# Optimization experiments

Measured on AMD Instinct MI355X. Metric: run time of the kernel, lower is better.

The kernel has to match this reference:

```python
import jax, jax.numpy as jnp
import numpy as np

N = 2000   # nodes
K = 16     # receptive-field size (exact degree incl. self-loop)
C_IN = 16  # input_feats
H = 16     # hidden_size
NC = 18    # num_contractions


def setup_inputs() -> dict:
    key = jax.random.key(0)
    k1, k2, k3, k4, k5, k6 = jax.random.split(key, 6)
    # adjacency with exactly K ones per row (self-loop + K-1 distinct random nbrs)
    u = jax.random.uniform(k1, (N, N))
    u = u.at[jnp.arange(N), jnp.arange(N)].set(-1.0)  # force self into top-K
    nbrs = jnp.argsort(u, axis=1)[:, :K]
    adj = jnp.zeros((N, N), jnp.float32).at[jnp.arange(N)[:, None], nbrs].set(1.0)
    X = jax.random.normal(k2, (N, C_IN), jnp.float32)
    scale = 0.1
    W1 = scale * jax.random.normal(k3, (H, NC * C_IN), jnp.float32)
    b1 = jnp.zeros((H,), jnp.float32)
    W2 = scale * jax.random.normal(k4, (H, NC * H), jnp.float32)
    b2 = jnp.zeros((H,), jnp.float32)
    fc_w = scale * jax.random.normal(k5, (1, 2 * H + C_IN), jnp.float32)
    fc_b = scale * jax.random.normal(k6, (1,), jnp.float32)
    return {"X": X, "adj": adj, "W1": W1, "b1": b1, "W2": W2, "b2": b2,
            "fc_w": fc_w, "fc_b": fc_b}


def _neighbors(adj):
    # each row has exactly K ones -> top_k returns their indices
    _, idx = jax.lax.top_k(adj, K)
    return jnp.sort(idx, axis=1)  # (N, K)


def _contract18(T):
    # T: (n, m, a, b, c) stacked promoted neighbor tensors; 18 contractions 3rd->2nd order
    n, k, _, _, c = T.shape
    tr = lambda M: jnp.swapaxes(M, 1, 2)
    s0, s1, s2 = T.sum(1), T.sum(2), T.sum(3)           # single-index sums
    d0 = jnp.einsum('ixxbc->ixbc', T)                    # diag m=a
    d1 = jnp.einsum('ixaxc->ixac', T)                    # diag m=b
    d2 = jnp.einsum('imyyc->imyc', T)                    # diag a=b
    outs = []
    for M in (s0, s1, s2, d0, d1, d2):
        outs.append(M)
        outs.append(tr(M))                               # 12 so far
    v0, v1, v2 = T.sum((2, 3)), T.sum((1, 3)), T.sum((1, 2))  # double sums -> vectors
    for v in (v0, v1, v2):
        outs.append(jnp.broadcast_to(v[:, :, None, :], (n, k, k, c)))  # rows
        outs.append(jnp.broadcast_to(v[:, None, :, :], (n, k, k, c)))  # cols
    return jnp.concatenate(outs, axis=-1)                # (n, k, k, 18c)


def _forward(X, adj, W1, b1, W2, b2, fc_w, fc_b):
    nbrs = _neighbors(adj)                               # (N, K)
    nbrs_nb = nbrs[nbrs]                                 # (N, K, K)
    # chi[i,m,a,b] = 1 iff a-th member of P_i equals b-th member of P_{nbrs[i,m]}
    chi = (nbrs[:, None, :, None] == nbrs_nb[:, :, None, :]).astype(X.dtype)  # (N,K,K,K)
    # F0: first->second order promotion (features on the diagonal of P_i x P_i)
    F0 = jnp.einsum('ab,iac->iabc', jnp.eye(K, dtype=X.dtype), X[nbrs])  # (N,K,K,C_IN)

    def step(F, W, b):
        Fn = F[nbrs]                                     # (N, m, p, q, c)
        tmp = jnp.einsum('imap,impqc->imaqc', chi, Fn)
        T = jnp.einsum('imaqc,imbq->imabc', tmp, chi)    # promoted + stacked (N,m,a,b,c)
        C = _contract18(T)                               # (N, a, b, 18c)
        return jax.nn.relu(jnp.einsum('iabk,hk->iabh', C, W) + b)

    F1 = step(F0, W1, b1)
    F2 = step(F1, W2, b2)
    g = jnp.concatenate([F0.sum((0, 1, 2)), F1.sum((0, 1, 2)), F2.sum((0, 1, 2))])
    return g @ fc_w.T + fc_b                             # (n_outputs,)


def reference(X, adj, W1, b1, W2, b2, fc_w, fc_b):
    return _forward(X, adj, W1, b1, W2, b2, fc_w, fc_b)
```

## Files before the change

kernel.cpp:

```cpp
#include <hip/hip_runtime.h>

#define NN 2000

typedef _Float16 halfx8 __attribute__((ext_vector_type(8)));
typedef float floatx4 __attribute__((ext_vector_type(4)));

#define LBAR() asm volatile("s_waitcnt lgkmcnt(0)\n\ts_barrier" ::: "memory")

__device__ __forceinline__ unsigned char to_fp8(float v) {
    return (unsigned char)(__builtin_amdgcn_cvt_pk_fp8_f32(v, 0.f, 0, false) & 0xff);
}

__global__ void build_nbrs_k(const float* __restrict__ adj,
                             int* __restrict__ nbrs,
                             float* __restrict__ gsum) {
    int i = blockIdx.x;
    int lane = threadIdx.x;
    if (i == 0 && lane == 0) {
        gsum[0] = 0.0f;
        ((unsigned*)gsum)[1] = 0u;
    }
    const float4* row = (const float4*)(adj + (size_t)i * NN);
    float4 v[8];
#pragma unroll
    for (int c = 0; c < 8; ++c) {
        int idx4 = c * 64 + lane;
        if (idx4 < 500) v[c] = row[idx4];
        else            v[c] = make_float4(0.f, 0.f, 0.f, 0.f);
    }
    int base = 0;
#pragma unroll
    for (int c = 0; c < 8; ++c) {
        unsigned nib = (v[c].x > 0.5f ? 1u : 0u) | (v[c].y > 0.5f ? 2u : 0u) |
                       (v[c].z > 0.5f ? 4u : 0u) | (v[c].w > 0.5f ? 8u : 0u);
        unsigned long long b0 = __ballot(nib & 1u);
        unsigned long long b1 = __ballot(nib & 2u);
        unsigned long long b2 = __ballot(nib & 4u);
        unsigned long long b3 = __ballot(nib & 8u);
        unsigned long long below = (1ull << lane) - 1ull;
        int pos = base + __popcll(b0 & below) + __popcll(b1 & below) +
                         __popcll(b2 & below) + __popcll(b3 & below);
        int col0 = c * 256 + lane * 4;
        if (nib & 1u) { nbrs[i * 16 + pos] = col0;     ++pos; }
        if (nib & 2u) { nbrs[i * 16 + pos] = col0 + 1; ++pos; }
        if (nib & 4u) { nbrs[i * 16 + pos] = col0 + 2; ++pos; }
        if (nib & 8u) { nbrs[i * 16 + pos] = col0 + 3; ++pos; }
        base += __popcll(b0) + __popcll(b1) + __popcll(b2) + __popcll(b3);
    }
}

__global__ void build_map_prep_k(const int* __restrict__ nbrs,
                                 signed char* __restrict__ map8,
                                 signed char* __restrict__ imp8,
                                 int4* __restrict__ aux,
                                 const float* __restrict__ W1,
                                 const float* __restrict__ W2,
                                 unsigned char* __restrict__ Wpk8,
                                 _Float16* __restrict__ Wpk16) {
    if (blockIdx.x >= 125) {
        int idx = (blockIdx.x - 125) * 256 + threadIdx.x;
        if (idx >= 10240) return;
        if (idx < 6144) {
            int stage = idx / 3072;
            int r = idx % 3072;
            int c = r / 512;
            int r2 = r % 512;
            int L = r2 >> 3, jj = r2 & 7;
            int q = L >> 4, h = L & 15;
            int k = q * 8 + jj;
            const int bA[6] = {2, 6, 10, 3, 7, 11};
            const int bB[6] = {4, 8, -1, 5, 9, -1};
            int tb = (k < 16) ? bA[c] : bB[c];
            int ci = k & 15;
            const float* W = stage ? W2 : W1;
            float val = (tb < 0) ? 0.f : W[h * 288 + tb * 16 + ci];
            Wpk8[idx] = to_fp8(val);
        } else {
            int id2 = idx - 6144;
            int stage = id2 / 2048;
            int r = id2 % 2048;
            int c = r / 512;
            int r2 = r % 512;
            int L = r2 >> 3, jj = r2 & 7;
            int q = L >> 4, h = L & 15;
            int k = q * 8 + jj;
            const int bA[4] = {0, 14, 1, 15};
            const int bB[4] = {12, 16, 13, 17};
            int tb = (k < 16) ? bA[c] : bB[c];
            int ci = k & 15;
            const float* W = stage ? W2 : W1;
            float val = W[h * 288 + tb * 16 + ci];
            Wpk16[id2] = (_Float16)val;
        }
        return;
    }
    int idx = blockIdx.x * 256 + threadIdx.x;
    if (idx >= NN * 16) return;
    int i = idx >> 4;
    int m = idx & 15;
    int j = nbrs[idx];
    const int4* pi = (const int4*)(nbrs + (size_t)i * 16);
    const int4* pj = (const int4*)(nbrs + (size_t)j * 16);
    int4 A = pi[0], Bq = pi[1], C = pi[2], D = pi[3];
    int4 E = pj[0], F = pj[1], G = pj[2], H = pj[3];
    int ni[16] = {A.x,A.y,A.z,A.w, Bq.x,Bq.y,Bq.z,Bq.w, C.x,C.y,C.z,C.w, D.x,D.y,D.z,D.w};
    int nj[16] = {E.x,E.y,E.z,E.w, F.x,F.y,F.z,F.w, G.x,G.y,G.z,G.w, H.x,H.y,H.z,H.w};

    int mp[16];
    unsigned long long lo = 0, hi = 0;
#pragma unroll
    for (int a = 0; a < 16; ++a) {
        int r = -1;
#pragma unroll
        for (int p = 0; p < 16; ++p)
            if (nj[p] == ni[a]) r = p;
        mp[a] = r;
        unsigned long long b = (unsigned long long)(r & 0xff);
        if (a < 8) lo |= b << (8 * a); else hi |= b << (8 * (a - 8));
    }
    uint4 pk;
    pk.x = (unsigned)lo; pk.y = (unsigned)(lo >> 32);
    pk.z = (unsigned)hi; pk.w = (unsigned)(hi >> 32);
    *(uint4*)(map8 + ((size_t)idx << 4)) = pk;
    lo = 0; hi = 0;
#pragma unroll
    for (int p = 0; p < 16; ++p) {
        int r = -1;
#pragma unroll
        for (int a = 0; a < 16; ++a)
            if (ni[a] == nj[p]) r = a;
        unsigned long long b = (unsigned long long)(r & 0xff);
        if (p < 8) lo |= b << (8 * p); else hi |= b << (8 * (p - 8));
    }
    pk.x = (unsigned)lo; pk.y = (unsigned)(lo >> 32);
    pk.z = (unsigned)hi; pk.w = (unsigned)(hi >> 32);
    *(uint4*)(imp8 + ((size_t)idx << 4)) = pk;

    unsigned vm = 0;
    int a1 = -1, a2 = -1, pa1 = 0, pa2 = 0;
#pragma unroll
    for (int a = 0; a < 16; ++a) {
        if (mp[a] >= 0) {
            vm |= (1u << a);
            if (a1 < 0)      { a1 = a; pa1 = mp[a]; }
            else if (a2 < 0) { a2 = a; pa2 = mp[a]; }
        }
    }
    int ms = 0;
#pragma unroll
    for (int a = 0; a < 16; ++a)
        if (ni[a] == i) ms = a;
    int4 av;
    av.x = j;
    av.y = (a1 & 0xff) | ((pa1 & 0xff) << 8) | ((a2 & 0xff) << 16) | ((pa2 & 0xff) << 24);
    av.z = (int)(vm | ((unsigned)(mp[m] & 0xff) << 16) | ((unsigned)(ms & 0xff) << 24));
    av.w = 0;
    aux[idx] = av;
}

template <int DIAG>
__global__ __launch_bounds__(256, 3)
void step_k(const float* __restrict__ Fp,
            const float* __restrict__ Xp,
            const unsigned char* __restrict__ Wpk8s,
            const _Float16* __restrict__ Wpk16s,
            const float* __restrict__ bias,
            const signed char* __restrict__ map8,
            const signed char* __restrict__ imp8,
            const int4* __restrict__ auxp,
            float* __restrict__ Fout,
            float* __restrict__ gp0,
            float* __restrict__ gp) {
    __shared__ __attribute__((aligned(16))) float S0[16][16][16];
    __shared__ __attribute__((aligned(16))) unsigned char MAP8[5][16][16][16];
    __shared__ __attribute__((aligned(16))) float V0f[16][16];
    __shared__ __attribute__((aligned(16))) float V1f[16][16];
    __shared__ __attribute__((aligned(16))) float V2f[16][16];
    __shared__ __attribute__((aligned(16))) float S1f[16][16];

    const int i = blockIdx.x;
    const int t = threadIdx.x;
    const int u = t >> 4;
    const int l = t & 15;
    const int lane = t & 63, q = lane >> 4, h = lane & 15, wv = t >> 6;

    int4 av = auxp[i * 16 + u];
    uint4 imv = *(const uint4*)(imp8 + ((size_t)(i * 16 + u) << 4));
    float bv = bias[l];
    const int j = av.x;
    const int a1 = (int)(signed char)(av.y & 0xff);
    const int pa1 = (av.y >> 8) & 0xff;
    const int a2 = (int)(signed char)((av.y >> 16) & 0xff);
    const int pa2 = (av.y >> 24) & 0xff;
    const unsigned vm = (unsigned)(av.z & 0xffff);
    const int pmm = (av.z >> 16) & 0xff;
    const int ms = (av.z >> 24) & 0xff;

    float frow[16], fcol[16], xv = 0.f;
    if (DIAG) {
        xv = Xp[(size_t)j * 16 + l];
    } else {
        const float* Fi = Fp + (size_t)i * 4096;
#pragma unroll
        for (int b = 0; b < 16; ++b) frow[b] = Fi[(u * 16 + b) * 16 + l];
#pragma unroll
        for (int a = 0; a < 16; ++a) fcol[a] = Fi[(a * 16 + u) * 16 + l];
    }

    float R1[16], R2[16];
    if (!DIAG && u != ms) {
        const float* P1 = Fp + (((size_t)j * 256 + pa1 * 16) * 16) + l;
#pragma unroll
        for (int p = 0; p < 16; ++p) R1[p] = P1[p * 16];
        if (a2 >= 0) {
            const float* P2 = Fp + (((size_t)j * 256 + pa2 * 16) * 16) + l;
#pragma unroll
            for (int p = 0; p < 16; ++p) R2[p] = P2[p * 16];
        }
    }
    long Bf8[6];
    {
        const long* Wq8 = (const long*)Wpk8s;
#pragma unroll
        for (int c = 0; c < 6; ++c) Bf8[c] = Wq8[c * 64 + lane];
    }
    halfx8 Bf16[4];
    {
        const halfx8* Wq16 = (const halfx8*)Wpk16s;
#pragma unroll
        for (int c = 0; c < 4; ++c) Bf16[c] = Wq16[c * 64 + lane];
    }

    if (u != ms) {
        uint4 z = {0u, 0u, 0u, 0u};
#pragma unroll
        for (int k = 0; k < 5; ++k)
            *(uint4*)&MAP8[k][u][l][0] = z;
    }
    if (DIAG) {
        S1f[u][l] = xv;
        V1f[u][l] = xv;
        V2f[u][l] = xv;
#pragma unroll
        for (int b = 0; b < 16; ++b) S0[u][b][l] = (b == u) ? xv : 0.f;
        unsigned char x8 = to_fp8(xv);
        MAP8[0][ms][u][l] = x8;
        MAP8[1][ms][u][l] = x8;
        unsigned char dz = (u == ms) ? x8 : (unsigned char)0;
        MAP8[2][ms][u][l] = dz;
        MAP8[3][ms][u][l] = dz;
        MAP8[4][ms][u][l] = x8;
    } else {
        float s2 = 0.f, a10 = 0.f, a8 = 0.f;
#pragma unroll
        for (int b = 0; b < 16; ++b) {
            float v = frow[b];
            s2 += v;
            S0[u][b][l] = v;
            if (b == u)  a10 = v;
            if (b == ms) a8 = v;
        }
        float s1 = 0.f, a6 = 0.f;
#pragma unroll
        for (int a = 0; a < 16; ++a) {
            float v = fcol[a];
            s1 += v;
            if (a == ms) a6 = v;
        }
        S1f[u][l] = s2;
        V1f[u][l] = s2;
        V2f[u][l] = s1;
        MAP8[0][ms][u][l] = to_fp8(s1);
        MAP8[1][ms][u][l] = to_fp8(s2);
        MAP8[2][ms][u][l] = to_fp8(a6);
        MAP8[3][ms][u][l] = to_fp8(a8);
        MAP8[4][ms][u][l] = to_fp8(a10);
    }
    LBAR();

    if (u != ms) {
        const int m = u;
        float v0acc = 0.f;
        if (DIAG) {
#pragma unroll
            for (int a = 0; a < 16; ++a) {
                if ((vm >> a) & 1u) {
                    float v = S1f[a][l];
                    v0acc += v;
                    atomicAdd(&S0[a][a][l], v);
                    atomicAdd(&V1f[a][l], v);
                    atomicAdd(&V2f[a][l], v);
                    unsigned char v8 = to_fp8(v);
                    MAP8[0][m][a][l] = v8;
                    MAP8[1][m][a][l] = v8;
                    MAP8[4][m][a][l] = v8;
                    if (a == m) { MAP8[2][m][m][l] = v8; MAP8[3][m][m][l] = v8; }
                }
            }
        } else {
            float colacc[16];
#pragma unroll
            for (int p = 0; p < 16; ++p) colacc[p] = 0.f;
            auto process = [&](int a, int pa, const float (&vr)[16]) {
                float rowacc = 0.f, a8v = 0.f, a10v = 0.f;
                const bool am = (a == m);
#pragma unroll
                for (int p = 0; p < 16; ++p) {
                    float v = vr[p];
                    if (p == pmm) a8v = v;
                    if (p == pa)  a10v = v;
                    unsigned dw = (p < 4) ? imv.x : ((p < 8) ? imv.y : ((p < 12) ? imv.z : imv.w));
                    int b = (int)(signed char)((dw >> (8 * (p & 3))) & 0xffu);
                    if (b >= 0) {
                        rowacc += v;
                        colacc[p] += v;
                        atomicAdd(&S0[a][b][l], v);
                        atomicAdd(&V2f[b][l], v);
                        if (am) MAP8[2][m][b][l] = to_fp8(v);
                    }
                }
                v0acc += rowacc;
                atomicAdd(&V1f[a][l], rowacc);
                MAP8[1][m][a][l] = to_fp8(rowacc);
                MAP8[3][m][a][l] = to_fp8(a8v);
                MAP8[4][m][a][l] = to_fp8(a10v);
            };
            process(a1, pa1, R1);
            if (a2 >= 0) process(a2, pa2, R2);
            unsigned rm = vm & ~(1u << a1);
            if (a2 >= 0) rm &= ~(1u << a2);
            if (rm) {
                uint4 mpq = *(const uint4*)(map8 + ((size_t)(i * 16 + u) << 4));
                do {
                    int a = __builtin_ctz(rm); rm &= rm - 1;
                    unsigned dw = (a & 8) ? ((a & 4) ? mpq.w : mpq.z) : ((a & 4) ? mpq.y : mpq.x);
                    int pa = (int)(signed char)((dw >> (8 * (a & 3))) & 0xffu);
                    float RT[16];
                    const float* P3 = Fp + (((size_t)j * 256 + pa * 16) * 16) + l;
#pragma unroll
                    for (int p = 0; p < 16; ++p) RT[p] = P3[p * 16];
                    process(a, pa, RT);
                } while (rm);
            }
#pragma unroll
            for (int p = 0; p < 16; ++p) {
                unsigned dw = (p < 4) ? imv.x : ((p < 8) ? imv.y : ((p < 12) ? imv.z : imv.w));
                int b = (int)(signed char)((dw >> (8 * (p & 3))) & 0xffu);
                if (b >= 0) MAP8[0][m][b][l] = to_fp8(colacc[p]);
            }
        }
        V0f[m][l] = v0acc;
    } else {
        float v0s = 0.f;
#pragma unroll
        for (int b = 0; b < 16; ++b) v0s += S1f[b][l];
        V0f[ms][l] = v0s;
        if (DIAG) gp0[l * 2048 + i] = v0s;
    }

    floatx4 acc1[4], acc2[4];
#pragma unroll
    for (int tt = 0; tt < 4; ++tt) {
        acc1[tt] = (floatx4){0.f, 0.f, 0.f, 0.f};
        acc2[tt] = (floatx4){0.f, 0.f, 0.f, 0.f};
    }
    const int wbase = wv * 4;
    {
        const int off8 = (q & 1) * 8;
        const unsigned char* mA = (q < 2) ? &MAP8[0][0][0][0] : &MAP8[1][0][0][0];
        const unsigned char* mB = (q < 2) ? &MAP8[2][0][0][0] : &MAP8[3][0][0][0];
        const unsigned char* mC = &MAP8[4][0][0][0];
#pragma unroll
        for (int tt = 0; tt < 4; ++tt) {
            const int x = wbase + tt;
            const int base = x * 256 + h * 16 + off8;
            long f0 = *(const long*)(mA + base);
            long f1 = *(const long*)(mB + base);
            long f2 = (q < 2) ? *(const long*)(mC + base) : 0L;
            acc1[tt] = __builtin_amdgcn_mfma_f32_16x16x32_fp8_fp8(f0, Bf8[0], acc1[tt], 0, 0, 0);
            acc1[tt] = __builtin_amdgcn_mfma_f32_16x16x32_fp8_fp8(f1, Bf8[1], acc1[tt], 0, 0, 0);
            acc1[tt] = __builtin_amdgcn_mfma_f32_16x16x32_fp8_fp8(f2, Bf8[2], acc1[tt], 0, 0, 0);
            acc2[tt] = __builtin_amdgcn_mfma_f32_16x16x32_fp8_fp8(f0, Bf8[3], acc2[tt], 0, 0, 0);
            acc2[tt] = __builtin_amdgcn_mfma_f32_16x16x32_fp8_fp8(f1, Bf8[4], acc2[tt], 0, 0, 0);
            acc2[tt] = __builtin_amdgcn_mfma_f32_16x16x32_fp8_fp8(f2, Bf8[5], acc2[tt], 0, 0, 0);
        }
    }
    LBAR();

    auto cvt8a = [](const float* p) -> halfx8 {
        float4 va = *(const float4*)p, vb = *(const float4*)(p + 4);
        halfx8 r;
        r[0] = (_Float16)va.x; r[1] = (_Float16)va.y; r[2] = (_Float16)va.z; r[3] = (_Float16)va.w;
        r[4] = (_Float16)vb.x; r[5] = (_Float16)vb.y; r[6] = (_Float16)vb.z; r[7] = (_Float16)vb.w;
        return r;
    };
#pragma unroll
    for (int tt = 0; tt < 4; ++tt) {
        const int x = wbase + tt;
        halfx8 p3, p4;
        if (q < 2) {
            p3 = cvt8a(&S0[x][h][q * 8]);
            p4 = cvt8a(&V1f[x][q * 8]);
        } else {
            const int c0 = (q - 2) * 8;
            p3 = cvt8a(&V0f[x][c0]);
            p4 = cvt8a(&V2f[x][c0]);
        }
        acc1[tt] = __builtin_amdgcn_mfma_f32_16x16x32_f16(p3, Bf16[0], acc1[tt], 0, 0, 0);
        acc1[tt] = __builtin_amdgcn_mfma_f32_16x16x32_f16(p4, Bf16[1], acc1[tt], 0, 0, 0);
        acc2[tt] = __builtin_amdgcn_mfma_f32_16x16x32_f16(p3, Bf16[2], acc2[tt], 0, 0, 0);
        acc2[tt] = __builtin_amdgcn_mfma_f32_16x16x32_f16(p4, Bf16[3], acc2[tt], 0, 0, 0);
    }

    float* P2f = (float*)&MAP8[0][0][0][0];
#pragma unroll
    for (int tt = 0; tt < 4; ++tt) {
        const int x = wbase + tt;
#pragma unroll
        for (int r = 0; r < 4; ++r)
            P2f[(x * 16 + (q * 4 + r)) * 17 + h] = acc2[tt][r];
    }
    LBAR();

    float gpart = 0.f;
#pragma unroll
    for (int tt = 0; tt < 4; ++tt) {
        const int x = wbase + tt;
#pragma unroll
        for (int r = 0; r < 4; ++r) {
            const int y = q * 4 + r;
            float val = acc1[tt][r] + P2f[(y * 16 + x) * 17 + h] + bv;
            val = fmaxf(val, 0.f);
            gpart += val;
            if (Fout) Fout[(size_t)i * 4096 + (x * 16 + y) * 16 + h] = val;
        }
    }
    gpart += __shfl_xor(gpart, 16, 64);
    gpart += __shfl_xor(gpart, 32, 64);
    if (lane < 16) gp[h * 8192 + i * 4 + wv] = gpart;
}

__global__ void reduce_fin_k(const float* __restrict__ parts,
                             float* __restrict__ gsum,
                             const float* __restrict__ fcw,
                             const float* __restrict__ fcb,
                             float* __restrict__ out) {
    int r = blockIdx.x;
    const float* p;
    int cnt4;
    if (r < 16)      { p = parts + r * 2048;                    cnt4 = 500;  }
    else if (r < 32) { p = parts + 32768 + (r - 16) * 8192;     cnt4 = 2000; }
    else             { p = parts + 163840 + (r - 32) * 8192;    cnt4 = 2000; }
    const float4* p4 = (const float4*)p;
    int t = threadIdx.x;
    float s = 0.f;
    for (int n = t; n < cnt4; n += 256) {
        float4 v = p4[n];
        s += v.x + v.y + v.z + v.w;
    }
#pragma unroll
    for (int off = 32; off > 0; off >>= 1) s += __shfl_xor(s, off, 64);
    __shared__ float wsum[4];
    if ((t & 63) == 0) wsum[t >> 6] = s;
    __syncthreads();
    if (t == 0) {
        float tot = wsum[0] + wsum[1] + wsum[2] + wsum[3];
        atomicAdd(&gsum[0], tot * fcw[r]);
        __threadfence();
        unsigned old = atomicAdd((unsigned*)gsum + 1, 1u);
        if (old == 47u) {
            float acc = atomicAdd(&gsum[0], 0.0f);
            out[0] = acc + fcb[0];
        }
    }
}

extern "C" void kernel_launch(void* const* d_in, const int* in_sizes, int n_in,
                              void* d_out, int out_size, void* d_ws, size_t ws_size,
                              hipStream_t stream) {
    const float* X   = (const float*)d_in[0];
    const float* adj = (const float*)d_in[1];
    const float* W1  = (const float*)d_in[2];
    const float* b1  = (const float*)d_in[3];
    const float* W2  = (const float*)d_in[4];
    const float* b2  = (const float*)d_in[5];
    const float* fcw = (const float*)d_in[6];
    const float* fcb = (const float*)d_in[7];
    float* out = (float*)d_out;
    char* ws = (char*)d_ws;

    float*         gsum  = (float*)(ws + 0);
    int*           nbrs  = (int*)(ws + 1024);
    signed char*   map8  = (signed char*)(ws + 129280);
    signed char*   imp8  = (signed char*)(ws + 641280);
    int4*          aux   = (int4*)(ws + 1153280);
    float*         parts = (float*)(ws + 1665280);
    unsigned char* Wpk8  = (unsigned char*)(ws + 2844928);
    _Float16*      Wpk16 = (_Float16*)(ws + 2851072);
    float*         F1    = (float*)(ws + 2859264);

    build_nbrs_k<<<NN, 64, 0, stream>>>(adj, nbrs, gsum);
    build_map_prep_k<<<165, 256, 0, stream>>>(nbrs, map8, imp8, aux, W1, W2, Wpk8, Wpk16);
    step_k<1><<<NN, 256, 0, stream>>>(nullptr, X, Wpk8, Wpk16, b1, map8, imp8, aux, F1,
                                      parts, parts + 32768);
    step_k<0><<<NN, 256, 0, stream>>>(F1, X, Wpk8 + 3072, Wpk16 + 2048, b2, map8, imp8, aux,
                                      nullptr, nullptr, parts + 163840);
    reduce_fin_k<<<48, 256, 0, stream>>>(parts, gsum, fcw, fcb, out);
}
```

Measured before the change: 145.9 us.

## Fold neighbor-map construction into step kernels and merge weight prep into nbrs kernel

Removes the separate map-building kernel. The weight-packing work moves into the adjacency-scan kernel as extra blocks, and each step kernel now computes its own neighbor-overlap maps (map, inverse map, first matches, self index) with wavefront ballots and shuffles. This saves one launch and the global writes and reads of the map8, imp8 and aux buffers. In exchange both step kernels redo the matching work and carry extra registers, which may affect occupancy under the launch bounds.

```diff
diff --git a/kernel.cpp b/kernel.cpp
--- a/kernel.cpp
+++ b/kernel.cpp
@@ -13,52 +13,15 @@
 
 __global__ void build_nbrs_k(const float* __restrict__ adj,
                              int* __restrict__ nbrs,
-                             float* __restrict__ gsum) {
+                             float* __restrict__ gsum,
+                             const float* __restrict__ W1,
+                             const float* __restrict__ W2,
+                             unsigned char* __restrict__ Wpk8,
+                             _Float16* __restrict__ Wpk16) {
     int i = blockIdx.x;
     int lane = threadIdx.x;
-    if (i == 0 && lane == 0) {
-        gsum[0] = 0.0f;
-        ((unsigned*)gsum)[1] = 0u;
-    }
-    const float4* row = (const float4*)(adj + (size_t)i * NN);
-    float4 v[8];
-#pragma unroll
-    for (int c = 0; c < 8; ++c) {
-        int idx4 = c * 64 + lane;
-        if (idx4 < 500) v[c] = row[idx4];
-        else            v[c] = make_float4(0.f, 0.f, 0.f, 0.f);
-    }
-    int base = 0;
-#pragma unroll
-    for (int c = 0; c < 8; ++c) {
-        unsigned nib = (v[c].x > 0.5f ? 1u : 0u) | (v[c].y > 0.5f ? 2u : 0u) |
-                       (v[c].z > 0.5f ? 4u : 0u) | (v[c].w > 0.5f ? 8u : 0u);
-        unsigned long long b0 = __ballot(nib & 1u);
-        unsigned long long b1 = __ballot(nib & 2u);
-        unsigned long long b2 = __ballot(nib & 4u);
-        unsigned long long b3 = __ballot(nib & 8u);
-        unsigned long long below = (1ull << lane) - 1ull;
-        int pos = base + __popcll(b0 & below) + __popcll(b1 & below) +
-                         __popcll(b2 & below) + __popcll(b3 & below);
-        int col0 = c * 256 + lane * 4;
-        if (nib & 1u) { nbrs[i * 16 + pos] = col0;     ++pos; }
-        if (nib & 2u) { nbrs[i * 16 + pos] = col0 + 1; ++pos; }
-        if (nib & 4u) { nbrs[i * 16 + pos] = col0 + 2; ++pos; }
-        if (nib & 8u) { nbrs[i * 16 + pos] = col0 + 3; ++pos; }
-        base += __popcll(b0) + __popcll(b1) + __popcll(b2) + __popcll(b3);
-    }
-}
-
-__global__ void build_map_prep_k(const int* __restrict__ nbrs,
-                                 signed char* __restrict__ map8,
-                                 signed char* __restrict__ imp8,
-                                 int4* __restrict__ aux,
-                                 const float* __restrict__ W1,
-                                 const float* __restrict__ W2,
-                                 unsigned char* __restrict__ Wpk8,
-                                 _Float16* __restrict__ Wpk16) {
-    if (blockIdx.x >= 125) {
-        int idx = (blockIdx.x - 125) * 256 + threadIdx.x;
+    if (i >= NN) {
+        int idx = (i - NN) * 64 + lane;
         if (idx >= 10240) return;
         if (idx < 6144) {
             int stage = idx / 3072;
@@ -94,68 +57,37 @@
         }
         return;
     }
-    int idx = blockIdx.x * 256 + threadIdx.x;
-    if (idx >= NN * 16) return;
-    int i = idx >> 4;
-    int m = idx & 15;
-    int j = nbrs[idx];
-    const int4* pi = (const int4*)(nbrs + (size_t)i * 16);
-    const int4* pj = (const int4*)(nbrs + (size_t)j * 16);
-    int4 A = pi[0], Bq = pi[1], C = pi[2], D = pi[3];
-    int4 E = pj[0], F = pj[1], G = pj[2], H = pj[3];
-    int ni[16] = {A.x,A.y,A.z,A.w, Bq.x,Bq.y,Bq.z,Bq.w, C.x,C.y,C.z,C.w, D.x,D.y,D.z,D.w};
-    int nj[16] = {E.x,E.y,E.z,E.w, F.x,F.y,F.z,F.w, G.x,G.y,G.z,G.w, H.x,H.y,H.z,H.w};
-
-    int mp[16];
-    unsigned long long lo = 0, hi = 0;
-#pragma unroll
-    for (int a = 0; a < 16; ++a) {
-        int r = -1;
-#pragma unroll
-        for (int p = 0; p < 16; ++p)
-            if (nj[p] == ni[a]) r = p;
-        mp[a] = r;
-        unsigned long long b = (unsigned long long)(r & 0xff);
-        if (a < 8) lo |= b << (8 * a); else hi |= b << (8 * (a - 8));
-    }
-    uint4 pk;
-    pk.x = (unsigned)lo; pk.y = (unsigned)(lo >> 32);
-    pk.z = (unsigned)hi; pk.w = (unsigned)(hi >> 32);
-    *(uint4*)(map8 + ((size_t)idx << 4)) = pk;
-    lo = 0; hi = 0;
-#pragma unroll
-    for (int p = 0; p < 16; ++p) {
-        int r = -1;
-#pragma unroll
-        for (int a = 0; a < 16; ++a)
-            if (ni[a] == nj[p]) r = a;
-        unsigned long long b = (unsigned long long)(r & 0xff);
-        if (p < 8) lo |= b << (8 * p); else hi |= b << (8 * (p - 8));
-    }
-    pk.x = (unsigned)lo; pk.y = (unsigned)(lo >> 32);
-    pk.z = (unsigned)hi; pk.w = (unsigned)(hi >> 32);
-    *(uint4*)(imp8 + ((size_t)idx << 4)) = pk;
-
-    unsigned vm = 0;
-    int a1 = -1, a2 = -1, pa1 = 0, pa2 = 0;
-#pragma unroll
-    for (int a = 0; a < 16; ++a) {
-        if (mp[a] >= 0) {
-            vm |= (1u << a);
-            if (a1 < 0)      { a1 = a; pa1 = mp[a]; }
-            else if (a2 < 0) { a2 = a; pa2 = mp[a]; }
-        }
-    }
-    int ms = 0;
-#pragma unroll
-    for (int a = 0; a < 16; ++a)
-        if (ni[a] == i) ms = a;
-    int4 av;
-    av.x = j;
-    av.y = (a1 & 0xff) | ((pa1 & 0xff) << 8) | ((a2 & 0xff) << 16) | ((pa2 & 0xff) << 24);
-    av.z = (int)(vm | ((unsigned)(mp[m] & 0xff) << 16) | ((unsigned)(ms & 0xff) << 24));
-    av.w = 0;
-    aux[idx] = av;
+    if (i == 0 && lane == 0) {
+        gsum[0] = 0.0f;
+        ((unsigned*)gsum)[1] = 0u;
+    }
+    const float4* row = (const float4*)(adj + (size_t)i * NN);
+    float4 v[8];
+#pragma unroll
+    for (int c = 0; c < 8; ++c) {
+        int idx4 = c * 64 + lane;
+        if (idx4 < 500) v[c] = row[idx4];
+        else            v[c] = make_float4(0.f, 0.f, 0.f, 0.f);
+    }
+    int base = 0;
+#pragma unroll
+    for (int c = 0; c < 8; ++c) {
+        unsigned nib = (v[c].x > 0.5f ? 1u : 0u) | (v[c].y > 0.5f ? 2u : 0u) |
+                       (v[c].z > 0.5f ? 4u : 0u) | (v[c].w > 0.5f ? 8u : 0u);
+        unsigned long long b0 = __ballot(nib & 1u);
+        unsigned long long b1 = __ballot(nib & 2u);
+        unsigned long long b2 = __ballot(nib & 4u);
+        unsigned long long b3 = __ballot(nib & 8u);
+        unsigned long long below = (1ull << lane) - 1ull;
+        int pos = base + __popcll(b0 & below) + __popcll(b1 & below) +
+                         __popcll(b2 & below) + __popcll(b3 & below);
+        int col0 = c * 256 + lane * 4;
+        if (nib & 1u) { nbrs[i * 16 + pos] = col0;     ++pos; }
+        if (nib & 2u) { nbrs[i * 16 + pos] = col0 + 1; ++pos; }
+        if (nib & 4u) { nbrs[i * 16 + pos] = col0 + 2; ++pos; }
+        if (nib & 8u) { nbrs[i * 16 + pos] = col0 + 3; ++pos; }
+        base += __popcll(b0) + __popcll(b1) + __popcll(b2) + __popcll(b3);
+    }
 }
 
 template <int DIAG>
@@ -165,9 +97,7 @@
             const unsigned char* __restrict__ Wpk8s,
             const _Float16* __restrict__ Wpk16s,
             const float* __restrict__ bias,
-            const signed char* __restrict__ map8,
-            const signed char* __restrict__ imp8,
-            const int4* __restrict__ auxp,
+            const int* __restrict__ nbrs,
             float* __restrict__ Fout,
             float* __restrict__ gp0,
             float* __restrict__ gp) {
@@ -183,18 +113,14 @@
     const int u = t >> 4;
     const int l = t & 15;
     const int lane = t & 63, q = lane >> 4, h = lane & 15, wv = t >> 6;
-
-    int4 av = auxp[i * 16 + u];
-    uint4 imv = *(const uint4*)(imp8 + ((size_t)(i * 16 + u) << 4));
+    const int gsh = lane & 48;
+
+    const int* nbi = nbrs + (size_t)i * 16;
+    const int j    = nbi[u];
+    const int ni_l = nbi[l];
+    int4 n0 = ((const int4*)nbi)[0], n1 = ((const int4*)nbi)[1],
+         n2 = ((const int4*)nbi)[2], n3 = ((const int4*)nbi)[3];
     float bv = bias[l];
-    const int j = av.x;
-    const int a1 = (int)(signed char)(av.y & 0xff);
-    const int pa1 = (av.y >> 8) & 0xff;
-    const int a2 = (int)(signed char)((av.y >> 16) & 0xff);
-    const int pa2 = (av.y >> 24) & 0xff;
-    const unsigned vm = (unsigned)(av.z & 0xffff);
-    const int pmm = (av.z >> 16) & 0xff;
-    const int ms = (av.z >> 24) & 0xff;
 
     float frow[16], fcol[16], xv = 0.f;
     if (DIAG) {
@@ -206,6 +132,65 @@
 #pragma unroll
         for (int a = 0; a < 16; ++a) fcol[a] = Fi[(a * 16 + u) * 16 + l];
     }
+    long Bf8[6];
+    {
+        const long* Wq8 = (const long*)Wpk8s;
+#pragma unroll
+        for (int c = 0; c < 6; ++c) Bf8[c] = Wq8[c * 64 + lane];
+    }
+    halfx8 Bf16[4];
+    {
+        const halfx8* Wq16 = (const halfx8*)Wpk16s;
+#pragma unroll
+        for (int c = 0; c < 4; ++c) Bf16[c] = Wq16[c * 64 + lane];
+    }
+    const int nj_l = nbrs[(size_t)j * 16 + l];
+
+    int ms = 0, a1 = -1, a2 = -1, pa1 = 0, pa2 = 0;
+    unsigned vm = 0, mpq0 = 0, mpq1 = 0, mpq2 = 0, mpq3 = 0;
+    {
+        const int niA[16] = {n0.x, n0.y, n0.z, n0.w, n1.x, n1.y, n1.z, n1.w,
+                             n2.x, n2.y, n2.z, n2.w, n3.x, n3.y, n3.z, n3.w};
+#pragma unroll
+        for (int a = 0; a < 16; ++a)
+            if (niA[a] == i) ms = a;
+#pragma unroll
+        for (int a = 0; a < 16; ++a) {
+            unsigned long long b = __ballot(nj_l == niA[a]);
+            unsigned gm = (unsigned)(b >> gsh) & 0xffffu;
+            unsigned pb = 0xffu;
+            if (gm) {
+                int p = __builtin_ctz(gm);
+                pb = (unsigned)p;
+                vm |= (1u << a);
+                if (a1 < 0)      { a1 = a; pa1 = p; }
+                else if (a2 < 0) { a2 = a; pa2 = p; }
+            }
+            unsigned sh = 8u * (a & 3);
+            if (a < 4)       mpq0 |= pb << sh;
+            else if (a < 8)  mpq1 |= pb << sh;
+            else if (a < 12) mpq2 |= pb << sh;
+            else             mpq3 |= pb << sh;
+        }
+    }
+    unsigned dwu = (u < 4) ? mpq0 : ((u < 8) ? mpq1 : ((u < 12) ? mpq2 : mpq3));
+    const int pmm = (int)((dwu >> (8 * (u & 3))) & 0xffu);
+
+    unsigned iv0 = 0, iv1 = 0, iv2 = 0, iv3 = 0;
+    if (!DIAG) {
+#pragma unroll
+        for (int p = 0; p < 16; ++p) {
+            int njp = __shfl(nj_l, gsh + p, 64);
+            unsigned long long b = __ballot(ni_l == njp);
+            unsigned gm = (unsigned)(b >> gsh) & 0xffffu;
+            unsigned ab = gm ? (unsigned)__builtin_ctz(gm) : 0xffu;
+            unsigned sh = 8u * (p & 3);
+            if (p < 4)       iv0 |= ab << sh;
+            else if (p < 8)  iv1 |= ab << sh;
+            else if (p < 12) iv2 |= ab << sh;
+            else             iv3 |= ab << sh;
+        }
+    }
 
     float R1[16], R2[16];
     if (!DIAG && u != ms) {
@@ -217,18 +202,6 @@
 #pragma unroll
             for (int p = 0; p < 16; ++p) R2[p] = P2[p * 16];
         }
-    }
-    long Bf8[6];
-    {
-        const long* Wq8 = (const long*)Wpk8s;
-#pragma unroll
-        for (int c = 0; c < 6; ++c) Bf8[c] = Wq8[c * 64 + lane];
-    }
-    halfx8 Bf16[4];
-    {
-        const halfx8* Wq16 = (const halfx8*)Wpk16s;
-#pragma unroll
-        for (int c = 0; c < 4; ++c) Bf16[c] = Wq16[c * 64 + lane];
     }
 
     if (u != ms) {
@@ -309,7 +282,7 @@
                     float v = vr[p];
                     if (p == pmm) a8v = v;
                     if (p == pa)  a10v = v;
-                    unsigned dw = (p < 4) ? imv.x : ((p < 8) ? imv.y : ((p < 12) ? imv.z : imv.w));
+                    unsigned dw = (p < 4) ? iv0 : ((p < 8) ? iv1 : ((p < 12) ? iv2 : iv3));
                     int b = (int)(signed char)((dw >> (8 * (p & 3))) & 0xffu);
                     if (b >= 0) {
                         rowacc += v;
@@ -330,11 +303,11 @@
             unsigned rm = vm & ~(1u << a1);
             if (a2 >= 0) rm &= ~(1u << a2);
             if (rm) {
-                uint4 mpq = *(const uint4*)(map8 + ((size_t)(i * 16 + u) << 4));
                 do {
                     int a = __builtin_ctz(rm); rm &= rm - 1;
-                    unsigned dw = (a & 8) ? ((a & 4) ? mpq.w : mpq.z) : ((a & 4) ? mpq.y : mpq.x);
-                    int pa = (int)(signed char)((dw >> (8 * (a & 3))) & 0xffu);
+                    unsigned dw2 = (a & 8) ? ((a & 4) ? mpq3 : mpq2)
+                                           : ((a & 4) ? mpq1 : mpq0);
+                    int pa = (int)(signed char)((dw2 >> (8 * (a & 3))) & 0xffu);
                     float RT[16];
                     const float* P3 = Fp + (((size_t)j * 256 + pa * 16) * 16) + l;
 #pragma unroll
@@ -344,7 +317,7 @@
             }
 #pragma unroll
             for (int p = 0; p < 16; ++p) {
-                unsigned dw = (p < 4) ? imv.x : ((p < 8) ? imv.y : ((p < 12) ? imv.z : imv.w));
+                unsigned dw = (p < 4) ? iv0 : ((p < 8) ? iv1 : ((p < 12) ? iv2 : iv3));
                 int b = (int)(signed char)((dw >> (8 * (p & 3))) & 0xffu);
                 if (b >= 0) MAP8[0][m][b][l] = to_fp8(colacc[p]);
             }
@@ -491,19 +464,15 @@
 
     float*         gsum  = (float*)(ws + 0);
     int*           nbrs  = (int*)(ws + 1024);
-    signed char*   map8  = (signed char*)(ws + 129280);
-    signed char*   imp8  = (signed char*)(ws + 641280);
-    int4*          aux   = (int4*)(ws + 1153280);
     float*         parts = (float*)(ws + 1665280);
     unsigned char* Wpk8  = (unsigned char*)(ws + 2844928);
     _Float16*      Wpk16 = (_Float16*)(ws + 2851072);
     float*         F1    = (float*)(ws + 2859264);
 
-    build_nbrs_k<<<NN, 64, 0, stream>>>(adj, nbrs, gsum);
-    build_map_prep_k<<<165, 256, 0, stream>>>(nbrs, map8, imp8, aux, W1, W2, Wpk8, Wpk16);
-    step_k<1><<<NN, 256, 0, stream>>>(nullptr, X, Wpk8, Wpk16, b1, map8, imp8, aux, F1,
+    build_nbrs_k<<<NN + 160, 64, 0, stream>>>(adj, nbrs, gsum, W1, W2, Wpk8, Wpk16);
+    step_k<1><<<NN, 256, 0, stream>>>(nullptr, X, Wpk8, Wpk16, b1, nbrs, F1,
                                       parts, parts + 32768);
-    step_k<0><<<NN, 256, 0, stream>>>(F1, X, Wpk8 + 3072, Wpk16 + 2048, b2, map8, imp8, aux,
+    step_k<0><<<NN, 256, 0, stream>>>(F1, X, Wpk8 + 3072, Wpk16 + 2048, b2, nbrs,
                                       nullptr, nullptr, parts + 163840);
     reduce_fin_k<<<48, 256, 0, stream>>>(parts, gsum, fcw, fcb, out);
 }
```

After: 144.0 us. No clear change (-1.3%).
